# Optimization experiments

Hardware: AMD Instinct MI355X
Metric: run time of the kernel (lower is better)

The kernel has to match this reference:

```python
import jax, jax.numpy as jnp
import numpy as np

B, NQ, N, D, H, R = 8, 64, 257, 768, 6, 64
DH = D // H  # 128
ALL_Q_MID = NQ * R  # 4096
LN_EPS = 1e-5


def setup_inputs() -> dict:
    key = jax.random.key(0)
    ks = jax.random.split(key, 7)
    s = 0.02
    return {
        "x": jax.random.normal(ks[0], (B, NQ, D), jnp.float32),
        "context": jax.random.normal(ks[1], (B, N, D), jnp.float32),
        "Wq": jax.random.normal(ks[2], (D, D), jnp.float32) * s,
        "Wk": jax.random.normal(ks[3], (D, D), jnp.float32) * s,
        "Wv1": jax.random.normal(ks[4], (ALL_Q_MID, D), jnp.float32) * s,
        "ln_g": jnp.ones((ALL_Q_MID,), jnp.float32),
        "ln_b": jnp.zeros((ALL_Q_MID,), jnp.float32),
        "Wconv": jax.random.normal(ks[5], (NQ, D, R), jnp.float32) * s,
        "Wout": jax.random.normal(ks[6], (D, D), jnp.float32) * s,
    }


def reference(x, context, Wq, Wk, Wv1, ln_g, ln_b, Wconv, Wout):
    b, nq, d = x.shape
    n = context.shape[1]
    dh = d // H

    # q, k projections, split heads: (b, h, len, dh)
    q = (x @ Wq.T).reshape(b, nq, H, dh).transpose(0, 2, 1, 3)
    k = (context @ Wk.T).reshape(b, n, H, dh).transpose(0, 2, 1, 3)

    # q-aware V: Linear -> LayerNorm(all_q_mid) -> grouped 1x1 conv (per-query lora expand)
    mid = context @ Wv1.T                                   # (b, n, NQ*R)
    mu = mid.mean(-1, keepdims=True)
    var = mid.var(-1, keepdims=True)
    mid = (mid - mu) * jax.lax.rsqrt(var + LN_EPS) * ln_g + ln_b
    midq = mid.reshape(b, n, NQ, -1)                        # (b, n, Q, r)
    v = jnp.einsum('bnqr,qdr->bqnd', midq, Wconv)           # per-query V: (b, Q, n, d)
    v = v.reshape(b, NQ, n, H, dh).transpose(0, 3, 1, 2, 4)  # (b, h, Q, n, dh)

    scale = dh ** (-0.25)
    sim = jnp.einsum('bhid,bhjd->bhij', q * scale, k * scale)  # (b, h, Q, n)
    attn = jax.nn.softmax(sim, axis=-1)
    # per-query value aggregation: attn[i, j] pairs with v[i, j, :]
    out = jnp.einsum('bhij,bhijd->bhid', attn, v)           # (b, h, Q, dh)
    out = out.transpose(0, 2, 1, 3).reshape(b, nq, d)       # (b, Q, d)
    return out @ Wout.T
```

## Files before the change

kernel.cpp:

```cpp
#include <hip/hip_runtime.h>

#define DEV __device__ __forceinline__

typedef __attribute__((ext_vector_type(8))) short sv8;
typedef __attribute__((ext_vector_type(4))) short sv4;
typedef __attribute__((ext_vector_type(4))) float f32x4;

DEV short f2bf(float f) {
  unsigned u = __float_as_uint(f);
  unsigned r = (u + 0x7fffu + ((u >> 16) & 1u)) >> 16;
  return (short)r;
}
DEV float bf2f(short s) {
  return __uint_as_float(((unsigned)(unsigned short)s) << 16);
}

DEV void gload16(const void* g, void* l) {
  __builtin_amdgcn_global_load_lds((const __attribute__((address_space(1))) void*)g,
                                   (__attribute__((address_space(3))) void*)l, 16, 0, 0);
}

struct Args {
  const float *x, *ctx, *Wq, *Wk, *Wv1, *ln_g, *ln_b, *Wconv, *Wout;
  short *x_bf, *ctx_bf, *wq_bf, *wk_bf, *wv1_bf, *wout_bf;
  short *q_bf, *k_bf, *mid_bf, *op_bf;
  float *attn, *stats, *tbuf, *out;
};

__global__ __launch_bounds__(256) void k_cvt(Args a) {
  const int gtid = blockIdx.x * 256 + threadIdx.x;
  const int T = gridDim.x * 256;
  for (int i = gtid; i < 1721856; i += T) {
    const float* s; short* d; int base;
    if      (i < 98304)   { s = a.x;    d = a.x_bf;    base = 0; }
    else if (i < 493056)  { s = a.ctx;  d = a.ctx_bf;  base = 98304; }
    else if (i < 640512)  { s = a.Wq;   d = a.wq_bf;   base = 493056; }
    else if (i < 787968)  { s = a.Wk;   d = a.wk_bf;   base = 640512; }
    else if (i < 1574400) { s = a.Wv1;  d = a.wv1_bf;  base = 787968; }
    else                  { s = a.Wout; d = a.wout_bf; base = 1574400; }
    int j = i - base;
    float4 v = ((const float4*)s)[j];
    sv4 o = { f2bf(v.x), f2bf(v.y), f2bf(v.z), f2bf(v.w) };
    ((sv4*)d)[j] = o;
  }
}

template <int MODE, int SPLITK>
DEV void gemm_tile(const short* __restrict__ A, const short* __restrict__ B,
                   void* __restrict__ C, int M, int N, int K,
                   int bm, int bn, int ks) {
  __shared__ __align__(16) short As[2][4096];
  __shared__ __align__(16) short Bs[2][4096];
  const int tid = threadIdx.x;
  const int wave = tid >> 6, lane = tid & 63;
  const int wr = wave >> 1, wc = wave & 1;
  const int row0 = bm * 128, col0 = bn * 128;
  const int rsel = lane & 15;
  const int Am = M - 1, Bm = N - 1;
  const int lr = lane >> 2;
  const int c8 = ((lane & 3) ^ ((lane >> 2) & 3)) * 8;
  const int Ksl = K / SPLITK;
  const int kbase = ks * Ksl;
  const int nt = Ksl / 32;

  const f32x4 z = {0.f, 0.f, 0.f, 0.f};
  f32x4 acc[4][4];
#pragma unroll
  for (int m = 0; m < 4; ++m)
#pragma unroll
    for (int n = 0; n < 4; ++n) acc[m][n] = z;

  auto stage = [&](int t, int buf) {
    int k0 = kbase + t * 32;
#pragma unroll
    for (int s = 0; s < 2; ++s) {
      int chunk = s * 4 + wave;
      int rr = chunk * 16 + lr;
      int gr = row0 + rr; if (gr > Am) gr = Am;
      gload16(A + (size_t)gr * K + k0 + c8, &As[buf][chunk * 512]);
      int gc = col0 + rr; if (gc > Bm) gc = Bm;
      gload16(B + (size_t)gc * K + k0 + c8, &Bs[buf][chunk * 512]);
    }
  };

  stage(0, 0);
  __syncthreads();
  const int ko = (((lane >> 4) ^ (rsel & 3)) * 8);

  for (int t = 0; t < nt; ++t) {
    int cur = t & 1;
    if (t + 1 < nt) stage(t + 1, cur ^ 1);
    sv8 a[4], b[4];
#pragma unroll
    for (int m = 0; m < 4; ++m)
      a[m] = *(const sv8*)(&As[cur][(wr * 64 + m * 16 + rsel) * 32 + ko]);
#pragma unroll
    for (int n = 0; n < 4; ++n)
      b[n] = *(const sv8*)(&Bs[cur][(wc * 64 + n * 16 + rsel) * 32 + ko]);
#pragma unroll
    for (int m = 0; m < 4; ++m)
#pragma unroll
      for (int n = 0; n < 4; ++n)
        acc[m][n] = __builtin_amdgcn_mfma_f32_16x16x32_bf16(a[m], b[n], acc[m][n], 0, 0, 0);
    __syncthreads();
  }

  const int cc = lane & 15, cr = (lane >> 4) * 4;
#pragma unroll
  for (int m = 0; m < 4; ++m)
#pragma unroll
    for (int n = 0; n < 4; ++n) {
      int c = col0 + wc * 64 + n * 16 + cc;
#pragma unroll
      for (int j = 0; j < 4; ++j) {
        int r = row0 + wr * 64 + m * 16 + cr + j;
        if (r < M && c < N) {
          float v = acc[m][n][j];
          if (MODE == 1) ((short*)C)[(size_t)r * N + c] = f2bf(v);
          else           atomicAdd(&((float*)C)[(size_t)r * N + c], v);
        }
      }
    }
}

__global__ __launch_bounds__(256) void k_gemm3(Args a) {
  const int bid = blockIdx.x;
  const short *A_, *B_; short* C_; int M_, nb_, local;
  if (bid < 24)       { A_ = a.x_bf;   B_ = a.wq_bf;  C_ = a.q_bf;   M_ = 512;  nb_ = 6;  local = bid; }
  else if (bid < 126) { A_ = a.ctx_bf; B_ = a.wk_bf;  C_ = a.k_bf;   M_ = 2056; nb_ = 6;  local = bid - 24; }
  else                { A_ = a.ctx_bf; B_ = a.wv1_bf; C_ = a.mid_bf; M_ = 2056; nb_ = 32; local = bid - 126; }
  gemm_tile<1, 1>(A_, B_, C_, M_, nb_ * 128, 768, local / nb_, local % nb_, 0);
}

DEV void attn_body(int bh, const short* __restrict__ qb, const short* __restrict__ kb,
                   float* __restrict__ attn, float (*wred)[64]) {
  const int b = bh / 6, h = bh % 6;
  const int tid = threadIdx.x, wave = tid >> 6, lane = tid & 63;
  const int rsel = lane & 15, koff = (lane >> 4) * 8;
  const int rhi = (lane >> 4) * 4;

  const f32x4 z = {0.f, 0.f, 0.f, 0.f};
  f32x4 acc[4][5];
#pragma unroll
  for (int m = 0; m < 4; ++m)
#pragma unroll
    for (int i = 0; i < 5; ++i) acc[m][i] = z;

#pragma unroll
  for (int k0 = 0; k0 < 128; k0 += 32) {
    sv8 a[4];
#pragma unroll
    for (int m = 0; m < 4; ++m)
      a[m] = *(const sv8*)(qb + (size_t)(b * 64 + m * 16 + rsel) * 768 + h * 128 + k0 + koff);
#pragma unroll
    for (int i = 0; i < 5; ++i) {
      int nf = wave + i * 4;
      if (nf > 16) continue;
      int j = nf * 16 + rsel; if (j > 256) j = 256;
      sv8 bf = *(const sv8*)(kb + (size_t)(b * 257 + j) * 768 + h * 128 + k0 + koff);
#pragma unroll
      for (int m = 0; m < 4; ++m)
        acc[m][i] = __builtin_amdgcn_mfma_f32_16x16x32_bf16(a[m], bf, acc[m][i], 0, 0, 0);
    }
  }
  const float S2 = 0.08838834764831845f;
#pragma unroll
  for (int m = 0; m < 4; ++m)
#pragma unroll
    for (int i = 0; i < 5; ++i) {
      int col = (wave + i * 4) * 16 + rsel;
      bool valid = col < 257;
#pragma unroll
      for (int j = 0; j < 4; ++j)
        acc[m][i][j] = valid ? acc[m][i][j] * S2 : -1e30f;
    }
  float mx[4][4];
#pragma unroll
  for (int m = 0; m < 4; ++m)
#pragma unroll
    for (int j = 0; j < 4; ++j) {
      float pm = acc[m][0][j];
#pragma unroll
      for (int i = 1; i < 5; ++i) pm = fmaxf(pm, acc[m][i][j]);
      pm = fmaxf(pm, __shfl_xor(pm, 1));
      pm = fmaxf(pm, __shfl_xor(pm, 2));
      pm = fmaxf(pm, __shfl_xor(pm, 4));
      pm = fmaxf(pm, __shfl_xor(pm, 8));
      mx[m][j] = pm;
      if (rsel == 0) wred[wave][m * 16 + rhi + j] = pm;
    }
  __syncthreads();
#pragma unroll
  for (int m = 0; m < 4; ++m)
#pragma unroll
    for (int j = 0; j < 4; ++j) {
      int row = m * 16 + rhi + j;
      mx[m][j] = fmaxf(fmaxf(wred[0][row], wred[1][row]), fmaxf(wred[2][row], wred[3][row]));
    }
  __syncthreads();
  float inv[4][4];
#pragma unroll
  for (int m = 0; m < 4; ++m)
#pragma unroll
    for (int j = 0; j < 4; ++j) {
      float ps = 0.f;
#pragma unroll
      for (int i = 0; i < 5; ++i) {
        float e = __expf(acc[m][i][j] - mx[m][j]);
        acc[m][i][j] = e;
        ps += e;
      }
      ps += __shfl_xor(ps, 1);
      ps += __shfl_xor(ps, 2);
      ps += __shfl_xor(ps, 4);
      ps += __shfl_xor(ps, 8);
      if (rsel == 0) wred[wave][m * 16 + rhi + j] = ps;
    }
  __syncthreads();
  float* base = attn + (size_t)bh * 64 * 257;
#pragma unroll
  for (int m = 0; m < 4; ++m)
#pragma unroll
    for (int j = 0; j < 4; ++j) {
      int row = m * 16 + rhi + j;
      float tot = wred[0][row] + wred[1][row] + wred[2][row] + wred[3][row];
      inv[m][j] = 1.f / tot;
    }
#pragma unroll
  for (int m = 0; m < 4; ++m)
#pragma unroll
    for (int i = 0; i < 5; ++i) {
      int nf = wave + i * 4;
      if (nf > 16) continue;
      int col = nf * 16 + rsel;
      if (col < 257) {
#pragma unroll
        for (int j = 0; j < 4; ++j)
          base[(size_t)(m * 16 + rhi + j) * 257 + col] = acc[m][i][j] * inv[m][j];
      }
    }
}

__global__ __launch_bounds__(256) void k_attn_stats(Args a) {
  __shared__ float wred[4][64];
  const int bid = blockIdx.x, tid = threadIdx.x;
  if (bid < 48) {
    attn_body(bid, a.q_bf, a.k_bf, a.attn, wred);
  } else if (bid < 305) {
    const int row = (bid - 48) * 8 + (tid >> 5);
    const int lane32 = tid & 31;
    const short* p = a.mid_bf + (size_t)row * 4096 + lane32 * 128;
    float s = 0.f, ss = 0.f;
#pragma unroll
    for (int i = 0; i < 16; ++i) {
      sv8 v = *(const sv8*)(p + i * 8);
#pragma unroll
      for (int j = 0; j < 8; ++j) { float f = bf2f(v[j]); s += f; ss += f * f; }
    }
#pragma unroll
    for (int off = 16; off; off >>= 1) { s += __shfl_xor(s, off); ss += __shfl_xor(ss, off); }
    if (lane32 == 0) {
      const float inv_n = 1.0f / 4096.0f;
      float mu = s * inv_n;
      float var = ss * inv_n - mu * mu;
      a.stats[row * 2]     = mu;
      a.stats[row * 2 + 1] = rsqrtf(var + 1e-5f);
    }
  } else {
    int i = (bid - 305) * 256 + tid;
    ((float4*)a.out)[i] = make_float4(0.f, 0.f, 0.f, 0.f);
  }
}

__global__ __launch_bounds__(256) void k_tk(Args a) {
  __shared__ short ms[257][64];
  __shared__ float w[6][257];
  __shared__ float mu[257], rs[257];
  __shared__ float redC[6][4], redS[6][4];
  const int bq = blockIdx.x;
  const int b = bq >> 6, q = bq & 63;
  const int tid = threadIdx.x, wave = tid >> 6;

  for (int lin = tid; lin < 257 * 8; lin += 256) {
    int j = lin >> 3, seg = (lin & 7) * 8;
    *(sv8*)(&ms[j][seg]) = *(const sv8*)(a.mid_bf + (size_t)(b * 257 + j) * 4096 + q * 64 + seg);
  }
  for (int j = tid; j < 257; j += 256) {
    mu[j] = a.stats[(b * 257 + j) * 2];
    rs[j] = a.stats[(b * 257 + j) * 2 + 1];
  }
  __syncthreads();

  float pc0[6] = {0.f, 0.f, 0.f, 0.f, 0.f, 0.f};
  float pS[6]  = {0.f, 0.f, 0.f, 0.f, 0.f, 0.f};
  for (int j = tid; j < 257; j += 256) {
    float rsj = rs[j], muj = mu[j];
#pragma unroll
    for (int h = 0; h < 6; ++h) {
      float av = a.attn[((size_t)(b * 6 + h) * 64 + q) * 257 + j];
      float wv = av * rsj;
      w[h][j] = wv;
      pS[h] += av;
      pc0[h] += wv * muj;
    }
  }
#pragma unroll
  for (int h = 0; h < 6; ++h) {
#pragma unroll
    for (int off = 32; off; off >>= 1) {
      pc0[h] += __shfl_xor(pc0[h], off);
      pS[h]  += __shfl_xor(pS[h], off);
    }
    if ((tid & 63) == 0) { redC[h][wave] = pc0[h]; redS[h][wave] = pS[h]; }
  }
  __syncthreads();

  for (int idx = tid; idx < 384; idx += 256) {
    const int h = idx >> 6, r = idx & 63;
    float s0 = 0.f, s1 = 0.f, s2 = 0.f, s3 = 0.f;
    for (int j = 0; j < 256; j += 4) {
      s0 += w[h][j]     * bf2f(ms[j][r]);
      s1 += w[h][j + 1] * bf2f(ms[j + 1][r]);
      s2 += w[h][j + 2] * bf2f(ms[j + 2][r]);
      s3 += w[h][j + 3] * bf2f(ms[j + 3][r]);
    }
    float stot = (s0 + s1) + (s2 + s3) + w[h][256] * bf2f(ms[256][r]);
    float c0 = redC[h][0] + redC[h][1] + redC[h][2] + redC[h][3];
    float S  = redS[h][0] + redS[h][1] + redS[h][2] + redS[h][3];
    float out = a.ln_g[q * 64 + r] * (stot - c0) + a.ln_b[q * 64 + r] * S;
    a.tbuf[((size_t)(b * 6 + h) * 64 + q) * 64 + r] = out;
  }
}

__global__ __launch_bounds__(256) void k_vproj(Args a) {
  __shared__ float ts[48][64];
  const int q = blockIdx.x / 3, chunk = blockIdx.x % 3;
  const int tid = threadIdx.x;
  for (int lin = tid; lin < 48 * 64; lin += 256) {
    int bh = lin >> 6, r = lin & 63;
    ts[bh][r] = a.tbuf[((size_t)bh * 64 + q) * 64 + r];
  }
  __syncthreads();
  const int d = chunk * 256 + tid;
  const int h = d >> 7;
  const float4* w4 = (const float4*)(a.Wconv + ((size_t)q * 768 + d) * 64);
  float acc[8] = {0.f, 0.f, 0.f, 0.f, 0.f, 0.f, 0.f, 0.f};
#pragma unroll
  for (int r4 = 0; r4 < 16; ++r4) {
    float4 wv = w4[r4];
#pragma unroll
    for (int bb = 0; bb < 8; ++bb) {
      acc[bb] += wv.x * ts[bb * 6 + h][r4 * 4 + 0];
      acc[bb] += wv.y * ts[bb * 6 + h][r4 * 4 + 1];
      acc[bb] += wv.z * ts[bb * 6 + h][r4 * 4 + 2];
      acc[bb] += wv.w * ts[bb * 6 + h][r4 * 4 + 3];
    }
  }
#pragma unroll
  for (int bb = 0; bb < 8; ++bb)
    a.op_bf[((size_t)(bb * 64 + q)) * 768 + d] = f2bf(acc[bb]);
}

__global__ __launch_bounds__(256) void k_outk(Args a) {
  gemm_tile<2, 4>(a.op_bf, a.wout_bf, a.out, 512, 768, 768,
                  blockIdx.x, blockIdx.y, blockIdx.z);
}

extern "C" void kernel_launch(void* const* d_in, const int* in_sizes, int n_in,
                              void* d_out, int out_size, void* d_ws, size_t ws_size,
                              hipStream_t stream) {
  (void)in_sizes; (void)n_in; (void)out_size; (void)ws_size;

  char* ws = (char*)d_ws;
  size_t off = 0;
  auto alloc = [&](size_t bytes) -> void* {
    void* p = (void*)(ws + off);
    off += (bytes + 255) & ~(size_t)255;
    return p;
  };

  Args a;
  a.x    = (const float*)d_in[0];
  a.ctx  = (const float*)d_in[1];
  a.Wq   = (const float*)d_in[2];
  a.Wk   = (const float*)d_in[3];
  a.Wv1  = (const float*)d_in[4];
  a.ln_g = (const float*)d_in[5];
  a.ln_b = (const float*)d_in[6];
  a.Wconv = (const float*)d_in[7];
  a.Wout = (const float*)d_in[8];
  a.out  = (float*)d_out;

  a.x_bf    = (short*)alloc((size_t)393216 * 2);
  a.ctx_bf  = (short*)alloc((size_t)1579008 * 2);
  a.wq_bf   = (short*)alloc((size_t)589824 * 2);
  a.wk_bf   = (short*)alloc((size_t)589824 * 2);
  a.wv1_bf  = (short*)alloc((size_t)3145728 * 2);
  a.wout_bf = (short*)alloc((size_t)589824 * 2);
  a.q_bf    = (short*)alloc((size_t)393216 * 2);
  a.k_bf    = (short*)alloc((size_t)1579008 * 2);
  a.mid_bf  = (short*)alloc((size_t)8421376 * 2);
  a.attn    = (float*)alloc((size_t)789504 * 4);
  a.stats   = (float*)alloc((size_t)4112 * 4);
  a.tbuf    = (float*)alloc((size_t)196608 * 4);
  a.op_bf   = (short*)alloc((size_t)393216 * 2);

  k_cvt<<<dim3(2048), dim3(256), 0, stream>>>(a);
  k_gemm3<<<dim3(670), dim3(256), 0, stream>>>(a);
  k_attn_stats<<<dim3(689), dim3(256), 0, stream>>>(a);
  k_tk<<<dim3(512), dim3(256), 0, stream>>>(a);
  k_vproj<<<dim3(192), dim3(256), 0, stream>>>(a);
  k_outk<<<dim3(4, 6, 4), dim3(256), 0, stream>>>(a);
}
```

Before: 172.5 us.

## Fuse LayerNorm stats into mid GEMM epilogue and attention softmax into tk kernel

The mid GEMM epilogue now writes per-64-column partial sums and sums of squares, which removes the separate pass that re-read mid_bf to compute LayerNorm statistics. The q·k scores and softmax are computed directly inside the per-(b,q) tk kernel with scalar dot products, so the attention kernel and its attn buffer round trip go away. Zeroing of the output moves into spare blocks of the vproj kernel. In exchange, the scores are recomputed with scalar FMAs instead of MFMA, each block reduces 64 partials per row, and the statistics use the E[x²]−μ² form on fp32 accumulators rather than on bf16 values.

```diff
diff --git a/kernel.cpp b/kernel.cpp
--- a/kernel.cpp
+++ b/kernel.cpp
@@ -24,7 +24,7 @@
   const float *x, *ctx, *Wq, *Wk, *Wv1, *ln_g, *ln_b, *Wconv, *Wout;
   short *x_bf, *ctx_bf, *wq_bf, *wk_bf, *wv1_bf, *wout_bf;
   short *q_bf, *k_bf, *mid_bf, *op_bf;
-  float *attn, *stats, *tbuf, *out;
+  float *psum, *psumsq, *tbuf, *out;
 };
 
 __global__ __launch_bounds__(256) void k_cvt(Args a) {
@@ -45,10 +45,11 @@
   }
 }
 
-template <int MODE, int SPLITK>
+template <int MODE, int SPLITK, int STATS>
 DEV void gemm_tile(const short* __restrict__ A, const short* __restrict__ B,
-                   void* __restrict__ C, int M, int N, int K,
-                   int bm, int bn, int ks) {
+                   void* __restrict__ C, float* __restrict__ psum,
+                   float* __restrict__ psumsq,
+                   int M, int N, int K, int bm, int bn, int ks) {
   __shared__ __align__(16) short As[2][4096];
   __shared__ __align__(16) short Bs[2][4096];
   const int tid = threadIdx.x;
@@ -121,198 +122,159 @@
         }
       }
     }
+
+  if (STATS) {
+#pragma unroll
+    for (int m = 0; m < 4; ++m)
+#pragma unroll
+      for (int j = 0; j < 4; ++j) {
+        float s = 0.f, s2 = 0.f;
+#pragma unroll
+        for (int n = 0; n < 4; ++n) { float v = acc[m][n][j]; s += v; s2 += v * v; }
+        s  += __shfl_xor(s, 1);  s2 += __shfl_xor(s2, 1);
+        s  += __shfl_xor(s, 2);  s2 += __shfl_xor(s2, 2);
+        s  += __shfl_xor(s, 4);  s2 += __shfl_xor(s2, 4);
+        s  += __shfl_xor(s, 8);  s2 += __shfl_xor(s2, 8);
+        int grow = row0 + wr * 64 + m * 16 + cr + j;
+        if ((lane & 15) == 0 && grow < M) {
+          int c64 = bn * 2 + wc;
+          psum[(size_t)c64 * M + grow]   = s;
+          psumsq[(size_t)c64 * M + grow] = s2;
+        }
+      }
+  }
 }
 
 __global__ __launch_bounds__(256) void k_gemm3(Args a) {
   const int bid = blockIdx.x;
-  const short *A_, *B_; short* C_; int M_, nb_, local;
-  if (bid < 24)       { A_ = a.x_bf;   B_ = a.wq_bf;  C_ = a.q_bf;   M_ = 512;  nb_ = 6;  local = bid; }
-  else if (bid < 126) { A_ = a.ctx_bf; B_ = a.wk_bf;  C_ = a.k_bf;   M_ = 2056; nb_ = 6;  local = bid - 24; }
-  else                { A_ = a.ctx_bf; B_ = a.wv1_bf; C_ = a.mid_bf; M_ = 2056; nb_ = 32; local = bid - 126; }
-  gemm_tile<1, 1>(A_, B_, C_, M_, nb_ * 128, 768, local / nb_, local % nb_, 0);
-}
-
-DEV void attn_body(int bh, const short* __restrict__ qb, const short* __restrict__ kb,
-                   float* __restrict__ attn, float (*wred)[64]) {
-  const int b = bh / 6, h = bh % 6;
-  const int tid = threadIdx.x, wave = tid >> 6, lane = tid & 63;
-  const int rsel = lane & 15, koff = (lane >> 4) * 8;
-  const int rhi = (lane >> 4) * 4;
-
-  const f32x4 z = {0.f, 0.f, 0.f, 0.f};
-  f32x4 acc[4][5];
-#pragma unroll
-  for (int m = 0; m < 4; ++m)
-#pragma unroll
-    for (int i = 0; i < 5; ++i) acc[m][i] = z;
-
-#pragma unroll
-  for (int k0 = 0; k0 < 128; k0 += 32) {
-    sv8 a[4];
-#pragma unroll
-    for (int m = 0; m < 4; ++m)
-      a[m] = *(const sv8*)(qb + (size_t)(b * 64 + m * 16 + rsel) * 768 + h * 128 + k0 + koff);
-#pragma unroll
-    for (int i = 0; i < 5; ++i) {
-      int nf = wave + i * 4;
-      if (nf > 16) continue;
-      int j = nf * 16 + rsel; if (j > 256) j = 256;
-      sv8 bf = *(const sv8*)(kb + (size_t)(b * 257 + j) * 768 + h * 128 + k0 + koff);
-#pragma unroll
-      for (int m = 0; m < 4; ++m)
-        acc[m][i] = __builtin_amdgcn_mfma_f32_16x16x32_bf16(a[m], bf, acc[m][i], 0, 0, 0);
-    }
-  }
-  const float S2 = 0.08838834764831845f;
-#pragma unroll
-  for (int m = 0; m < 4; ++m)
-#pragma unroll
-    for (int i = 0; i < 5; ++i) {
-      int col = (wave + i * 4) * 16 + rsel;
-      bool valid = col < 257;
-#pragma unroll
-      for (int j = 0; j < 4; ++j)
-        acc[m][i][j] = valid ? acc[m][i][j] * S2 : -1e30f;
-    }
-  float mx[4][4];
-#pragma unroll
-  for (int m = 0; m < 4; ++m)
-#pragma unroll
-    for (int j = 0; j < 4; ++j) {
-      float pm = acc[m][0][j];
-#pragma unroll
-      for (int i = 1; i < 5; ++i) pm = fmaxf(pm, acc[m][i][j]);
-      pm = fmaxf(pm, __shfl_xor(pm, 1));
-      pm = fmaxf(pm, __shfl_xor(pm, 2));
-      pm = fmaxf(pm, __shfl_xor(pm, 4));
-      pm = fmaxf(pm, __shfl_xor(pm, 8));
-      mx[m][j] = pm;
-      if (rsel == 0) wred[wave][m * 16 + rhi + j] = pm;
-    }
-  __syncthreads();
-#pragma unroll
-  for (int m = 0; m < 4; ++m)
-#pragma unroll
-    for (int j = 0; j < 4; ++j) {
-      int row = m * 16 + rhi + j;
-      mx[m][j] = fmaxf(fmaxf(wred[0][row], wred[1][row]), fmaxf(wred[2][row], wred[3][row]));
-    }
-  __syncthreads();
-  float inv[4][4];
-#pragma unroll
-  for (int m = 0; m < 4; ++m)
-#pragma unroll
-    for (int j = 0; j < 4; ++j) {
-      float ps = 0.f;
-#pragma unroll
-      for (int i = 0; i < 5; ++i) {
-        float e = __expf(acc[m][i][j] - mx[m][j]);
-        acc[m][i][j] = e;
-        ps += e;
-      }
-      ps += __shfl_xor(ps, 1);
-      ps += __shfl_xor(ps, 2);
-      ps += __shfl_xor(ps, 4);
-      ps += __shfl_xor(ps, 8);
-      if (rsel == 0) wred[wave][m * 16 + rhi + j] = ps;
-    }
-  __syncthreads();
-  float* base = attn + (size_t)bh * 64 * 257;
-#pragma unroll
-  for (int m = 0; m < 4; ++m)
-#pragma unroll
-    for (int j = 0; j < 4; ++j) {
-      int row = m * 16 + rhi + j;
-      float tot = wred[0][row] + wred[1][row] + wred[2][row] + wred[3][row];
-      inv[m][j] = 1.f / tot;
-    }
-#pragma unroll
-  for (int m = 0; m < 4; ++m)
-#pragma unroll
-    for (int i = 0; i < 5; ++i) {
-      int nf = wave + i * 4;
-      if (nf > 16) continue;
-      int col = nf * 16 + rsel;
-      if (col < 257) {
-#pragma unroll
-        for (int j = 0; j < 4; ++j)
-          base[(size_t)(m * 16 + rhi + j) * 257 + col] = acc[m][i][j] * inv[m][j];
-      }
-    }
-}
-
-__global__ __launch_bounds__(256) void k_attn_stats(Args a) {
-  __shared__ float wred[4][64];
-  const int bid = blockIdx.x, tid = threadIdx.x;
-  if (bid < 48) {
-    attn_body(bid, a.q_bf, a.k_bf, a.attn, wred);
-  } else if (bid < 305) {
-    const int row = (bid - 48) * 8 + (tid >> 5);
-    const int lane32 = tid & 31;
-    const short* p = a.mid_bf + (size_t)row * 4096 + lane32 * 128;
-    float s = 0.f, ss = 0.f;
-#pragma unroll
-    for (int i = 0; i < 16; ++i) {
-      sv8 v = *(const sv8*)(p + i * 8);
-#pragma unroll
-      for (int j = 0; j < 8; ++j) { float f = bf2f(v[j]); s += f; ss += f * f; }
-    }
-#pragma unroll
-    for (int off = 16; off; off >>= 1) { s += __shfl_xor(s, off); ss += __shfl_xor(ss, off); }
-    if (lane32 == 0) {
-      const float inv_n = 1.0f / 4096.0f;
-      float mu = s * inv_n;
-      float var = ss * inv_n - mu * mu;
-      a.stats[row * 2]     = mu;
-      a.stats[row * 2 + 1] = rsqrtf(var + 1e-5f);
-    }
+  if (bid < 24) {
+    gemm_tile<1, 1, 0>(a.x_bf, a.wq_bf, a.q_bf, nullptr, nullptr,
+                       512, 768, 768, bid / 6, bid % 6, 0);
+  } else if (bid < 126) {
+    int local = bid - 24;
+    gemm_tile<1, 1, 0>(a.ctx_bf, a.wk_bf, a.k_bf, nullptr, nullptr,
+                       2056, 768, 768, local / 6, local % 6, 0);
   } else {
-    int i = (bid - 305) * 256 + tid;
-    ((float4*)a.out)[i] = make_float4(0.f, 0.f, 0.f, 0.f);
-  }
-}
-
-__global__ __launch_bounds__(256) void k_tk(Args a) {
+    int local = bid - 126;
+    gemm_tile<1, 1, 1>(a.ctx_bf, a.wv1_bf, a.mid_bf, a.psum, a.psumsq,
+                       2056, 4096, 768, local / 32, local % 32, 0);
+  }
+}
+
+__global__ __launch_bounds__(256) void k_tk2(Args a) {
   __shared__ short ms[257][64];
+  __shared__ float qv[6][128];
   __shared__ float w[6][257];
-  __shared__ float mu[257], rs[257];
-  __shared__ float redC[6][4], redS[6][4];
+  __shared__ float muld[257], rsld[257];
+  __shared__ float wredA[6][4], wredB[6][4];
+  __shared__ float c0sh[6], dinv[6];
   const int bq = blockIdx.x;
   const int b = bq >> 6, q = bq & 63;
-  const int tid = threadIdx.x, wave = tid >> 6;
+  const int tid = threadIdx.x, wave = tid >> 6, lane = tid & 63;
+  const float S2 = 0.08838834764831845f;
 
   for (int lin = tid; lin < 257 * 8; lin += 256) {
     int j = lin >> 3, seg = (lin & 7) * 8;
     *(sv8*)(&ms[j][seg]) = *(const sv8*)(a.mid_bf + (size_t)(b * 257 + j) * 4096 + q * 64 + seg);
   }
+  for (int i = tid; i < 768; i += 256)
+    qv[i >> 7][i & 127] = bf2f(a.q_bf[(size_t)(b * 64 + q) * 768 + i]);
   for (int j = tid; j < 257; j += 256) {
-    mu[j] = a.stats[(b * 257 + j) * 2];
-    rs[j] = a.stats[(b * 257 + j) * 2 + 1];
-  }
-  __syncthreads();
-
-  float pc0[6] = {0.f, 0.f, 0.f, 0.f, 0.f, 0.f};
-  float pS[6]  = {0.f, 0.f, 0.f, 0.f, 0.f, 0.f};
+    int grow = b * 257 + j;
+    float s = 0.f, s2 = 0.f;
+#pragma unroll 8
+    for (int c = 0; c < 64; ++c) {
+      s  += a.psum[(size_t)c * 2056 + grow];
+      s2 += a.psumsq[(size_t)c * 2056 + grow];
+    }
+    float mu = s * (1.0f / 4096.0f);
+    float var = s2 * (1.0f / 4096.0f) - mu * mu;
+    muld[j] = mu;
+    rsld[j] = rsqrtf(var + 1e-5f);
+  }
+  __syncthreads();
+
   for (int j = tid; j < 257; j += 256) {
-    float rsj = rs[j], muj = mu[j];
+    const short* kr = a.k_bf + (size_t)(b * 257 + j) * 768;
+    float acc6[6];
 #pragma unroll
     for (int h = 0; h < 6; ++h) {
-      float av = a.attn[((size_t)(b * 6 + h) * 64 + q) * 257 + j];
-      float wv = av * rsj;
+      float s = 0.f;
+#pragma unroll
+      for (int db = 0; db < 16; ++db) {
+        sv8 kk = *(const sv8*)(kr + h * 128 + db * 8);
+        const float4* qp = (const float4*)&qv[h][db * 8];
+        float4 q0 = qp[0], q1 = qp[1];
+        s += q0.x * bf2f(kk[0]); s += q0.y * bf2f(kk[1]);
+        s += q0.z * bf2f(kk[2]); s += q0.w * bf2f(kk[3]);
+        s += q1.x * bf2f(kk[4]); s += q1.y * bf2f(kk[5]);
+        s += q1.z * bf2f(kk[6]); s += q1.w * bf2f(kk[7]);
+      }
+      acc6[h] = s * S2;
+    }
+#pragma unroll
+    for (int h = 0; h < 6; ++h) w[h][j] = acc6[h];
+  }
+
+  float p[6];
+#pragma unroll
+  for (int h = 0; h < 6; ++h) p[h] = -1e30f;
+  for (int j = tid; j < 257; j += 256)
+#pragma unroll
+    for (int h = 0; h < 6; ++h) p[h] = fmaxf(p[h], w[h][j]);
+#pragma unroll
+  for (int h = 0; h < 6; ++h) {
+#pragma unroll
+    for (int off = 32; off; off >>= 1) p[h] = fmaxf(p[h], __shfl_xor(p[h], off));
+    if (lane == 0) wredA[h][wave] = p[h];
+  }
+  __syncthreads();
+  float mx[6];
+#pragma unroll
+  for (int h = 0; h < 6; ++h)
+    mx[h] = fmaxf(fmaxf(wredA[h][0], wredA[h][1]), fmaxf(wredA[h][2], wredA[h][3]));
+  __syncthreads();
+
+#pragma unroll
+  for (int h = 0; h < 6; ++h) p[h] = 0.f;
+  for (int j = tid; j < 257; j += 256)
+#pragma unroll
+    for (int h = 0; h < 6; ++h) {
+      float e = __expf(w[h][j] - mx[h]);
+      w[h][j] = e;
+      p[h] += e;
+    }
+#pragma unroll
+  for (int h = 0; h < 6; ++h) {
+#pragma unroll
+    for (int off = 32; off; off >>= 1) p[h] += __shfl_xor(p[h], off);
+    if (lane == 0) wredB[h][wave] = p[h];
+  }
+  __syncthreads();
+  if (tid < 6)
+    dinv[tid] = 1.f / (wredB[tid][0] + wredB[tid][1] + wredB[tid][2] + wredB[tid][3]);
+  __syncthreads();
+
+#pragma unroll
+  for (int h = 0; h < 6; ++h) p[h] = 0.f;
+  for (int j = tid; j < 257; j += 256) {
+    float rsj = rsld[j], muj = muld[j];
+#pragma unroll
+    for (int h = 0; h < 6; ++h) {
+      float wv = w[h][j] * dinv[h] * rsj;
       w[h][j] = wv;
-      pS[h] += av;
-      pc0[h] += wv * muj;
+      p[h] += wv * muj;
     }
   }
 #pragma unroll
   for (int h = 0; h < 6; ++h) {
 #pragma unroll
-    for (int off = 32; off; off >>= 1) {
-      pc0[h] += __shfl_xor(pc0[h], off);
-      pS[h]  += __shfl_xor(pS[h], off);
-    }
-    if ((tid & 63) == 0) { redC[h][wave] = pc0[h]; redS[h][wave] = pS[h]; }
-  }
+    for (int off = 32; off; off >>= 1) p[h] += __shfl_xor(p[h], off);
+    if (lane == 0) wredA[h][wave] = p[h];
+  }
+  __syncthreads();
+  if (tid < 6)
+    c0sh[tid] = wredA[tid][0] + wredA[tid][1] + wredA[tid][2] + wredA[tid][3];
   __syncthreads();
 
   for (int idx = tid; idx < 384; idx += 256) {
@@ -325,17 +287,20 @@
       s3 += w[h][j + 3] * bf2f(ms[j + 3][r]);
     }
     float stot = (s0 + s1) + (s2 + s3) + w[h][256] * bf2f(ms[256][r]);
-    float c0 = redC[h][0] + redC[h][1] + redC[h][2] + redC[h][3];
-    float S  = redS[h][0] + redS[h][1] + redS[h][2] + redS[h][3];
-    float out = a.ln_g[q * 64 + r] * (stot - c0) + a.ln_b[q * 64 + r] * S;
+    float out = a.ln_g[q * 64 + r] * (stot - c0sh[h]) + a.ln_b[q * 64 + r];
     a.tbuf[((size_t)(b * 6 + h) * 64 + q) * 64 + r] = out;
   }
 }
 
 __global__ __launch_bounds__(256) void k_vproj(Args a) {
+  const int bid = blockIdx.x, tid = threadIdx.x;
+  if (bid >= 192) {
+    int i = (bid - 192) * 256 + tid;
+    ((float4*)a.out)[i] = make_float4(0.f, 0.f, 0.f, 0.f);
+    return;
+  }
   __shared__ float ts[48][64];
-  const int q = blockIdx.x / 3, chunk = blockIdx.x % 3;
-  const int tid = threadIdx.x;
+  const int q = bid / 3, chunk = bid % 3;
   for (int lin = tid; lin < 48 * 64; lin += 256) {
     int bh = lin >> 6, r = lin & 63;
     ts[bh][r] = a.tbuf[((size_t)bh * 64 + q) * 64 + r];
@@ -362,8 +327,8 @@
 }
 
 __global__ __launch_bounds__(256) void k_outk(Args a) {
-  gemm_tile<2, 4>(a.op_bf, a.wout_bf, a.out, 512, 768, 768,
-                  blockIdx.x, blockIdx.y, blockIdx.z);
+  gemm_tile<2, 4, 0>(a.op_bf, a.wout_bf, a.out, nullptr, nullptr,
+                     512, 768, 768, blockIdx.x, blockIdx.y, blockIdx.z);
 }
 
 extern "C" void kernel_launch(void* const* d_in, const int* in_sizes, int n_in,
@@ -400,15 +365,14 @@
   a.q_bf    = (short*)alloc((size_t)393216 * 2);
   a.k_bf    = (short*)alloc((size_t)1579008 * 2);
   a.mid_bf  = (short*)alloc((size_t)8421376 * 2);
-  a.attn    = (float*)alloc((size_t)789504 * 4);
-  a.stats   = (float*)alloc((size_t)4112 * 4);
+  a.psum    = (float*)alloc((size_t)64 * 2056 * 4);
+  a.psumsq  = (float*)alloc((size_t)64 * 2056 * 4);
   a.tbuf    = (float*)alloc((size_t)196608 * 4);
   a.op_bf   = (short*)alloc((size_t)393216 * 2);
 
   k_cvt<<<dim3(2048), dim3(256), 0, stream>>>(a);
   k_gemm3<<<dim3(670), dim3(256), 0, stream>>>(a);
-  k_attn_stats<<<dim3(689), dim3(256), 0, stream>>>(a);
-  k_tk<<<dim3(512), dim3(256), 0, stream>>>(a);
-  k_vproj<<<dim3(192), dim3(256), 0, stream>>>(a);
+  k_tk2<<<dim3(512), dim3(256), 0, stream>>>(a);
+  k_vproj<<<dim3(576), dim3(256), 0, stream>>>(a);
   k_outk<<<dim3(4, 6, 4), dim3(256), 0, stream>>>(a);
 }
```

Measured after the change: 265.2 us. +53.7%, slower.
